# Performance work log

Measured on AMD Instinct MI355X. Metric: run time of the kernel, lower is better.

The kernel has to match this reference:

```python
import math
import jax, jax.numpy as jnp
import numpy as np

_TEMP_CLAMP = 4.6

def _l2n(x):
    # torch F.normalize: x / max(||x||, eps)
    return x / jnp.maximum(jnp.linalg.norm(x, axis=-1, keepdims=True), 1e-12)

def setup_inputs() -> dict:
    key = jax.random.key(0)
    k1, k2, k3, k4, k5 = jax.random.split(key, 5)
    B, S, D, V, NNEG = 1024, 64, 128, 100000, 2048
    hidden = jax.random.normal(k1, (B, S, D), dtype=jnp.float32)
    y = jax.random.randint(k2, (B, S), 0, V, dtype=jnp.int64)
    embed_table = jax.random.normal(k3, (V, D), dtype=jnp.float32)
    sampling_probs = jax.random.uniform(k4, (V,), dtype=jnp.float32, minval=1e-6, maxval=1.0)
    sampled_indices = jax.random.randint(k5, (NNEG,), 0, V, dtype=jnp.int64)
    log_temperature = jnp.asarray(math.log(1.0 / 0.07), dtype=jnp.float32)
    return {"hidden": hidden, "y": y, "embed_table": embed_table,
            "sampling_probs": sampling_probs, "sampled_indices": sampled_indices,
            "log_temperature": log_temperature}

def reference(hidden, y, embed_table, sampling_probs, sampled_indices, log_temperature):
    D = hidden.shape[-1]
    h = hidden.reshape(-1, D)          # [N, D]
    yf = y.reshape(-1)                 # [N]
    valid = (yf != 0)                  # padding mask (static-shape weighting instead of boolean gather)

    true_p = sampling_probs[yf]                # [N]
    samp_p = sampling_probs[sampled_indices]   # [NNEG]
    e_pos = embed_table[yf]                    # [N, D]
    e_neg = embed_table[sampled_indices]       # [NNEG, D]

    temp = jnp.exp(jnp.minimum(log_temperature, _TEMP_CLAMP))
    hn = _l2n(h)
    pos_logits = jnp.sum(hn * _l2n(e_pos), axis=-1) * temp        # [N]
    neg_logits = (hn @ _l2n(e_neg).T) * temp                      # [N, NNEG]

    collision = yf[:, None] == sampled_indices[None, :]
    neg_logits = jnp.where(collision, -1e9, neg_logits)

    pos_adj = pos_logits - jnp.log(true_p + 1e-10)                # [N]
    neg_adj = neg_logits - jnp.log(samp_p + 1e-10)[None, :]       # [N, NNEG]
    logits = jnp.concatenate([pos_adj[:, None], neg_adj], axis=1) # [N, 1+NNEG]

    per_row = -jax.nn.log_softmax(logits, axis=-1)[:, 0]          # CE with label 0
    w = valid.astype(per_row.dtype)
    return jnp.sum(per_row * w) / jnp.maximum(jnp.sum(w), 1.0)
```

## Files before the change

### kernel.cpp

```cpp
#include <hip/hip_runtime.h>
#include <math.h>

#define TPB 256
#define NNEG 2048
#define D 128
#define RPB 128
#define RPW 32
#define NSPLIT 2
#define HALF (NNEG / NSPLIT)
#define NCHH (HALF / 64)
#define L2E 1.44269504088896340736f

typedef __attribute__((ext_vector_type(8))) short bf16x8;
typedef __attribute__((ext_vector_type(4))) float f32x4;

#define MFMA16 __builtin_amdgcn_mfma_f32_16x16x32_bf16

static __device__ __forceinline__ unsigned int f2bf(float f) {
    unsigned int u = __float_as_uint(f);
    return (u + 0x7FFFu + ((u >> 16) & 1u)) >> 16;
}

static __device__ __forceinline__ void stage16(const void* g, void* l) {
    __builtin_amdgcn_global_load_lds(
        (const __attribute__((address_space(1))) unsigned int*)g,
        (__attribute__((address_space(3))) unsigned int*)l, 16, 0, 0);
}

__global__ __launch_bounds__(TPB) void sspe_prep(
    const float* __restrict__ embed,
    const float* __restrict__ sprobs,
    const int* __restrict__ sidx,
    unsigned int* __restrict__ en_bf,
    float* __restrict__ ln_samp)
{
    const int t = threadIdx.x;
    const int wave = t >> 6;
    const int lane = t & 63;
    const int j = blockIdx.x * 4 + wave;
    const int idx = sidx[j];

    float2 v = reinterpret_cast<const float2*>(embed)[(size_t)idx * 64 + lane];
    float ss = v.x * v.x + v.y * v.y;
    ss += __shfl_xor(ss, 1);
    ss += __shfl_xor(ss, 2);
    ss += __shfl_xor(ss, 4);
    ss += __shfl_xor(ss, 8);
    ss += __shfl_xor(ss, 16);
    ss += __shfl_xor(ss, 32);
    const float rinv = 1.0f / fmaxf(sqrtf(ss), 1e-12f);
    en_bf[(size_t)j * 64 + lane] = f2bf(v.x * rinv) | (f2bf(v.y * rinv) << 16);
    if (lane == 0) ln_samp[j] = logf(sprobs[idx] + 1e-10f);
}

__global__ __launch_bounds__(TPB, 4) void sspe_main(
    const float* __restrict__ hidden,
    const int* __restrict__ y,
    const float* __restrict__ embed,
    const float* __restrict__ sprobs,
    const int* __restrict__ sidx,
    const float* __restrict__ ltemp,
    const unsigned int* __restrict__ en_bf,
    const float* __restrict__ ln_samp,
    float* __restrict__ pos_adj,
    float* __restrict__ lsum,
    int nrows)
{
    const int t = threadIdx.x;
    const int wave = t >> 6;
    const int lane = t & 63;
    const int jh = blockIdx.x & 1;
    const int rb = (blockIdx.x >> 1) * RPB;

    __shared__ __align__(16) unsigned char smem[RPB * 256];
    __shared__ int ys[RPB];

    const float temp = __builtin_amdgcn_exp2f(fminf(ltemp[0], 4.6f) * L2E);
    const float t2 = temp * L2E;
    const float Mln = temp + 14.0f;
    const float M2 = Mln * L2E;

    if (t < RPB) ys[t] = y[rb + t];
    __syncthreads();

    #pragma unroll 1
    for (int i = 0; i < RPW; i += 4) {
        float2 h2[4], e2[4];
        int yi[4];
        #pragma unroll
        for (int u = 0; u < 4; ++u) {
            const int lr = wave * RPW + i + u;
            h2[u] = reinterpret_cast<const float2*>(hidden)[(size_t)(rb + lr) * 64 + lane];
            yi[u] = ys[lr];
            e2[u] = make_float2(0.0f, 0.0f);
        }
        if (jh == 0) {
            #pragma unroll
            for (int u = 0; u < 4; ++u)
                e2[u] = reinterpret_cast<const float2*>(embed)[(size_t)yi[u] * 64 + lane];
        }
        float ss[4], es[4], dt[4];
        #pragma unroll
        for (int u = 0; u < 4; ++u) {
            ss[u] = h2[u].x * h2[u].x + h2[u].y * h2[u].y;
            es[u] = e2[u].x * e2[u].x + e2[u].y * e2[u].y;
            dt[u] = h2[u].x * e2[u].x + h2[u].y * e2[u].y;
        }
        #pragma unroll
        for (int m = 1; m <= 32; m <<= 1)
            #pragma unroll
            for (int u = 0; u < 4; ++u) {
                ss[u] += __shfl_xor(ss[u], m);
                es[u] += __shfl_xor(es[u], m);
                dt[u] += __shfl_xor(dt[u], m);
            }
        #pragma unroll
        for (int u = 0; u < 4; ++u) {
            const int lr = wave * RPW + i + u;
            const float rinv = 1.0f / fmaxf(sqrtf(ss[u]), 1e-12f);
            const unsigned int uu = f2bf(h2[u].x * rinv) | (f2bf(h2[u].y * rinv) << 16);
            const int rx = (lr & 7) << 4;
            *reinterpret_cast<unsigned int*>(smem + lr * 256 + ((lane * 4) ^ rx)) = uu;
            if (jh == 0 && lane == 0)
                pos_adj[rb + lr] = dt[u] * rinv * (1.0f / fmaxf(sqrtf(es[u]), 1e-12f)) * temp
                                   - logf(sprobs[yi[u]] + 1e-10f);
        }
    }
    __syncthreads();

    bf16x8 A0[4], A1[4];
    {
        const int row0 = wave * RPW + (lane & 15);
        const int rx = (lane & 7) << 4;
        #pragma unroll
        for (int ks = 0; ks < 4; ++ks) {
            const int col = (ks * 64 + ((lane >> 4) << 4)) ^ rx;
            A0[ks] = *reinterpret_cast<const bf16x8*>(smem + row0 * 256 + col);
            A1[ks] = *reinterpret_cast<const bf16x8*>(smem + (row0 + 16) * 256 + col);
        }
    }
    __syncthreads();

    const int cj = lane & 15;
    const int rgrp = lane >> 4;
    int yv0[4], yv1[4];
    float l0[4], l1[4];
    #pragma unroll
    for (int j = 0; j < 4; ++j) {
        yv0[j] = ys[wave * RPW + rgrp * 4 + j];
        yv1[j] = ys[wave * RPW + 16 + rgrp * 4 + j];
        l0[j] = 0.0f;
        l1[j] = 0.0f;
    }

    unsigned int soff[4];
    #pragma unroll
    for (int i = 0; i < 4; ++i) {
        const int d = wave * 4 + i;
        soff[i] = (unsigned int)((d >> 2) * 4096 + (lane & 15) * 256
                                 + (d & 3) * 64 + (lane >> 4) * 16);
    }
    const unsigned char* en = reinterpret_cast<const unsigned char*>(en_bf)
                            + (size_t)jh * HALF * 256;
    const int nb0 = jh * HALF;

    #pragma unroll
    for (int i = 0; i < 4; ++i)
        stage16(en + soff[i], smem + (wave * 4 + i) * 1024);

    #pragma unroll 1
    for (int ch = 0; ch < NCHH; ++ch) {
        const int cur = (ch & 1) << 14;
        __syncthreads();

        float lk[4];
        int ci[4];
        #pragma unroll
        for (int nt = 0; nt < 4; ++nt) {
            lk[nt] = ln_samp[nb0 + ch * 64 + nt * 16 + cj];
            ci[nt] = sidx[nb0 + ch * 64 + nt * 16 + cj];
        }

        if (ch + 1 < NCHH) {
            const unsigned char* enn = en + (size_t)(ch + 1) * 16384;
            #pragma unroll
            for (int i = 0; i < 4; ++i)
                stage16(enn + soff[i], smem + (cur ^ 16384) + (wave * 4 + i) * 1024);
        }

        const unsigned char* bb = smem + cur + lane * 16;
        f32x4 c0[4], c1[4];
        #pragma unroll
        for (int nt = 0; nt < 4; ++nt) {
            c0[nt] = (f32x4){0.f, 0.f, 0.f, 0.f};
            c1[nt] = (f32x4){0.f, 0.f, 0.f, 0.f};
            #pragma unroll
            for (int ks = 0; ks < 4; ++ks) {
                const bf16x8 b = *reinterpret_cast<const bf16x8*>(bb + (nt * 4 + ks) * 1024);
                c0[nt] = MFMA16(A0[ks], b, c0[nt], 0, 0, 0);
                c1[nt] = MFMA16(A1[ks], b, c1[nt], 0, 0, 0);
            }
        }

        #pragma unroll
        for (int nt = 0; nt < 4; ++nt) {
            const float nl2 = fmaf(lk[nt], -L2E, -M2);
            #pragma unroll
            for (int j = 0; j < 4; ++j) {
                const float a0 = fmaf(c0[nt][j], t2, nl2);
                const float a1 = fmaf(c1[nt][j], t2, nl2);
                const float e0 = __builtin_amdgcn_exp2f(a0);
                const float e1 = __builtin_amdgcn_exp2f(a1);
                l0[j] += (ci[nt] == yv0[j]) ? 0.0f : e0;
                l1[j] += (ci[nt] == yv1[j]) ? 0.0f : e1;
            }
        }
    }

    #pragma unroll
    for (int j = 0; j < 4; ++j) {
        float v0 = l0[j], v1 = l1[j];
        v0 += __shfl_xor(v0, 1);  v1 += __shfl_xor(v1, 1);
        v0 += __shfl_xor(v0, 2);  v1 += __shfl_xor(v1, 2);
        v0 += __shfl_xor(v0, 4);  v1 += __shfl_xor(v1, 4);
        v0 += __shfl_xor(v0, 8);  v1 += __shfl_xor(v1, 8);
        l0[j] = v0;
        l1[j] = v1;
    }
    if (cj == 0) {
        float* dst = lsum + (size_t)jh * nrows + rb + wave * RPW;
        #pragma unroll
        for (int j = 0; j < 4; ++j) {
            dst[rgrp * 4 + j] = l0[j];
            dst[16 + rgrp * 4 + j] = l1[j];
        }
    }
}

__global__ __launch_bounds__(TPB) void sspe_rows(
    const int* __restrict__ y,
    const float* __restrict__ ltemp,
    const float* __restrict__ pos_adj,
    const float* __restrict__ lsum,
    int nrows,
    float2* __restrict__ partials)
{
    __shared__ float2 red2[4];
    const int t = threadIdx.x;
    const int wave = t >> 6;
    const int lane = t & 63;
    const int r = blockIdx.x * TPB + t;

    const float temp = __builtin_amdgcn_exp2f(fminf(ltemp[0], 4.6f) * L2E);
    const float Mln = temp + 14.0f;
    const float M2 = Mln * L2E;

    const float s = lsum[r] + lsum[(size_t)nrows + r];
    const float pa = pos_adj[r];
    const float stot = s + __builtin_amdgcn_exp2f(fmaf(pa, L2E, -M2));
    float w = (y[r] != 0) ? 1.0f : 0.0f;
    float per = (Mln + logf(stot) - pa) * w;

    #pragma unroll
    for (int msk = 1; msk < 64; msk <<= 1) {
        per += __shfl_xor(per, msk);
        w += __shfl_xor(w, msk);
    }
    if (lane == 0) red2[wave] = make_float2(per, w);
    __syncthreads();
    if (t == 0) {
        const float2 a = red2[0], b = red2[1], c = red2[2], d = red2[3];
        partials[blockIdx.x] = make_float2(a.x + b.x + c.x + d.x,
                                           a.y + b.y + c.y + d.y);
    }
}

__global__ __launch_bounds__(TPB) void sspe_finalize(
    const float2* __restrict__ partials, int n, float* __restrict__ out)
{
    __shared__ float ssum[TPB];
    __shared__ float scnt[TPB];
    const int t = threadIdx.x;
    float s = 0.0f, c = 0.0f;
    for (int i = t; i < n; i += TPB) {
        const float2 p = partials[i];
        s += p.x; c += p.y;
    }
    ssum[t] = s; scnt[t] = c;
    __syncthreads();
    for (int k = TPB / 2; k > 0; k >>= 1) {
        if (t < k) { ssum[t] += ssum[t + k]; scnt[t] += scnt[t + k]; }
        __syncthreads();
    }
    if (t == 0) out[0] = ssum[0] / fmaxf(scnt[0], 1.0f);
}

extern "C" void kernel_launch(void* const* d_in, const int* in_sizes, int n_in,
                              void* d_out, int out_size, void* d_ws, size_t ws_size,
                              hipStream_t stream) {
    const float* hidden = (const float*)d_in[0];
    const int*   yv     = (const int*)d_in[1];
    const float* embed  = (const float*)d_in[2];
    const float* sprobs = (const float*)d_in[3];
    const int*   sidx   = (const int*)d_in[4];
    const float* ltemp  = (const float*)d_in[5];
    float* out = (float*)d_out;

    const int nrows = in_sizes[1];
    const int nblocks = (nrows / RPB) * NSPLIT;

    char* w = (char*)d_ws;
    size_t off = 0;
    unsigned int* en_bf = (unsigned int*)(w + off); off += (size_t)NNEG * D * 2;
    float* ln_samp      = (float*)(w + off);        off += (size_t)NNEG * 4;
    float* pos_adj      = (float*)(w + off);        off += (size_t)nrows * 4;
    float* lsum         = (float*)(w + off);        off += (size_t)NSPLIT * nrows * 4;
    float2* partials    = (float2*)(w + off);

    sspe_prep<<<NNEG / 4, TPB, 0, stream>>>(embed, sprobs, sidx, en_bf, ln_samp);
    sspe_main<<<nblocks, TPB, 0, stream>>>(hidden, yv, embed, sprobs, sidx, ltemp,
                                           en_bf, ln_samp, pos_adj, lsum, nrows);
    sspe_rows<<<nrows / TPB, TPB, 0, stream>>>(yv, ltemp, pos_adj, lsum, nrows, partials);
    sspe_finalize<<<1, TPB, 0, stream>>>(partials, nrows / TPB, out);
}
```

Baseline: 93.72 us.

## Move collision masking out of main GEMM loop via bitmap-driven correction pass

The main kernel stops comparing every label against every sampled index inside the exp-sum loop. Instead, the prep kernel builds a vocab bitmap of the sampled ids, and the rows kernel recomputes and subtracts the contribution of colliding negatives for the few rows that hit. The main kernel also changes its tiling: 256 rows per block and a 4-way split of the negatives. Each wave now normalizes hidden rows directly into MFMA registers, without an LDS round-trip, and holds four 16-row A tiles. Costs are an extra clear kernel, an atomic bitmap build and per-row correction work, plus a clamp that guards against cancellation error.

```diff
diff --git a/kernel.cpp b/kernel.cpp
--- a/kernel.cpp
+++ b/kernel.cpp
@@ -4,11 +4,10 @@
 #define TPB 256
 #define NNEG 2048
 #define D 128
-#define RPB 128
-#define RPW 32
-#define NSPLIT 2
-#define HALF (NNEG / NSPLIT)
-#define NCHH (HALF / 64)
+#define RPB 256
+#define NSPLIT 4
+#define QSZ (NNEG / NSPLIT)
+#define NCHQ (QSZ / 64)
 #define L2E 1.44269504088896340736f
 
 typedef __attribute__((ext_vector_type(8))) short bf16x8;
@@ -19,12 +18,24 @@
 static __device__ __forceinline__ unsigned int f2bf(float f) {
     unsigned int u = __float_as_uint(f);
     return (u + 0x7FFFu + ((u >> 16) & 1u)) >> 16;
+}
+static __device__ __forceinline__ float bfround(float f) {
+    unsigned int u = __float_as_uint(f);
+    return __uint_as_float((u + 0x7FFFu + ((u >> 16) & 1u)) & 0xFFFF0000u);
+}
+static __device__ __forceinline__ unsigned int pk2(float x, float y) {
+    return f2bf(x) | (f2bf(y) << 16);
 }
 
 static __device__ __forceinline__ void stage16(const void* g, void* l) {
     __builtin_amdgcn_global_load_lds(
         (const __attribute__((address_space(1))) unsigned int*)g,
         (__attribute__((address_space(3))) unsigned int*)l, 16, 0, 0);
+}
+
+__global__ __launch_bounds__(TPB) void sspe_clear(unsigned int* __restrict__ bm, int words) {
+    const int i = blockIdx.x * TPB + threadIdx.x;
+    if (i < words) bm[i] = 0u;
 }
 
 __global__ __launch_bounds__(TPB) void sspe_prep(
@@ -32,7 +43,8 @@
     const float* __restrict__ sprobs,
     const int* __restrict__ sidx,
     unsigned int* __restrict__ en_bf,
-    float* __restrict__ ln_samp)
+    float* __restrict__ ln_samp,
+    unsigned int* __restrict__ bitmap)
 {
     const int t = threadIdx.x;
     const int wave = t >> 6;
@@ -49,8 +61,11 @@
     ss += __shfl_xor(ss, 16);
     ss += __shfl_xor(ss, 32);
     const float rinv = 1.0f / fmaxf(sqrtf(ss), 1e-12f);
-    en_bf[(size_t)j * 64 + lane] = f2bf(v.x * rinv) | (f2bf(v.y * rinv) << 16);
-    if (lane == 0) ln_samp[j] = logf(sprobs[idx] + 1e-10f);
+    en_bf[(size_t)j * 64 + lane] = pk2(v.x * rinv, v.y * rinv);
+    if (lane == 0) {
+        ln_samp[j] = logf(sprobs[idx] + 1e-10f);
+        atomicOr(&bitmap[idx >> 5], 1u << (idx & 31));
+    }
 }
 
 __global__ __launch_bounds__(TPB, 4) void sspe_main(
@@ -58,7 +73,6 @@
     const int* __restrict__ y,
     const float* __restrict__ embed,
     const float* __restrict__ sprobs,
-    const int* __restrict__ sidx,
     const float* __restrict__ ltemp,
     const unsigned int* __restrict__ en_bf,
     const float* __restrict__ ln_samp,
@@ -69,119 +83,106 @@
     const int t = threadIdx.x;
     const int wave = t >> 6;
     const int lane = t & 63;
-    const int jh = blockIdx.x & 1;
-    const int rb = (blockIdx.x >> 1) * RPB;
-
-    __shared__ __align__(16) unsigned char smem[RPB * 256];
-    __shared__ int ys[RPB];
+    const int jh = blockIdx.x & 3;
+    const int rb = (blockIdx.x >> 2) * RPB;
+
+    __shared__ __align__(16) unsigned char smem[2 * 16384];
 
     const float temp = __builtin_amdgcn_exp2f(fminf(ltemp[0], 4.6f) * L2E);
     const float t2 = temp * L2E;
     const float Mln = temp + 14.0f;
     const float M2 = Mln * L2E;
 
-    if (t < RPB) ys[t] = y[rb + t];
-    __syncthreads();
-
-    #pragma unroll 1
-    for (int i = 0; i < RPW; i += 4) {
-        float2 h2[4], e2[4];
-        int yi[4];
-        #pragma unroll
-        for (int u = 0; u < 4; ++u) {
-            const int lr = wave * RPW + i + u;
-            h2[u] = reinterpret_cast<const float2*>(hidden)[(size_t)(rb + lr) * 64 + lane];
-            yi[u] = ys[lr];
-            e2[u] = make_float2(0.0f, 0.0f);
-        }
-        if (jh == 0) {
-            #pragma unroll
-            for (int u = 0; u < 4; ++u)
-                e2[u] = reinterpret_cast<const float2*>(embed)[(size_t)yi[u] * 64 + lane];
-        }
-        float ss[4], es[4], dt[4];
-        #pragma unroll
-        for (int u = 0; u < 4; ++u) {
-            ss[u] = h2[u].x * h2[u].x + h2[u].y * h2[u].y;
-            es[u] = e2[u].x * e2[u].x + e2[u].y * e2[u].y;
-            dt[u] = h2[u].x * e2[u].x + h2[u].y * e2[u].y;
-        }
-        #pragma unroll
-        for (int m = 1; m <= 32; m <<= 1)
-            #pragma unroll
-            for (int u = 0; u < 4; ++u) {
-                ss[u] += __shfl_xor(ss[u], m);
-                es[u] += __shfl_xor(es[u], m);
-                dt[u] += __shfl_xor(dt[u], m);
-            }
-        #pragma unroll
-        for (int u = 0; u < 4; ++u) {
-            const int lr = wave * RPW + i + u;
-            const float rinv = 1.0f / fmaxf(sqrtf(ss[u]), 1e-12f);
-            const unsigned int uu = f2bf(h2[u].x * rinv) | (f2bf(h2[u].y * rinv) << 16);
-            const int rx = (lr & 7) << 4;
-            *reinterpret_cast<unsigned int*>(smem + lr * 256 + ((lane * 4) ^ rx)) = uu;
-            if (jh == 0 && lane == 0)
-                pos_adj[rb + lr] = dt[u] * rinv * (1.0f / fmaxf(sqrtf(es[u]), 1e-12f)) * temp
-                                   - logf(sprobs[yi[u]] + 1e-10f);
-        }
-    }
-    __syncthreads();
-
-    bf16x8 A0[4], A1[4];
-    {
-        const int row0 = wave * RPW + (lane & 15);
-        const int rx = (lane & 7) << 4;
-        #pragma unroll
-        for (int ks = 0; ks < 4; ++ks) {
-            const int col = (ks * 64 + ((lane >> 4) << 4)) ^ rx;
-            A0[ks] = *reinterpret_cast<const bf16x8*>(smem + row0 * 256 + col);
-            A1[ks] = *reinterpret_cast<const bf16x8*>(smem + (row0 + 16) * 256 + col);
-        }
-    }
-    __syncthreads();
-
-    const int cj = lane & 15;
-    const int rgrp = lane >> 4;
-    int yv0[4], yv1[4];
-    float l0[4], l1[4];
-    #pragma unroll
-    for (int j = 0; j < 4; ++j) {
-        yv0[j] = ys[wave * RPW + rgrp * 4 + j];
-        yv1[j] = ys[wave * RPW + 16 + rgrp * 4 + j];
-        l0[j] = 0.0f;
-        l1[j] = 0.0f;
-    }
+    const int g = lane >> 4;
+    const int rl = lane & 15;
+    const int wbase = rb + wave * 64;
 
     unsigned int soff[4];
     #pragma unroll
     for (int i = 0; i < 4; ++i) {
         const int d = wave * 4 + i;
-        soff[i] = (unsigned int)((d >> 2) * 4096 + (lane & 15) * 256
-                                 + (d & 3) * 64 + (lane >> 4) * 16);
+        soff[i] = (unsigned int)((d >> 2) * 4096 + rl * 256 + (d & 3) * 64 + g * 16);
     }
     const unsigned char* en = reinterpret_cast<const unsigned char*>(en_bf)
-                            + (size_t)jh * HALF * 256;
-    const int nb0 = jh * HALF;
+                            + (size_t)jh * QSZ * 256;
+    const int nb0 = jh * QSZ;
 
     #pragma unroll
     for (int i = 0; i < 4; ++i)
         stage16(en + soff[i], smem + (wave * 4 + i) * 1024);
 
+    bf16x8 A[4][4];
+    #pragma unroll
+    for (int tt = 0; tt < 4; ++tt) {
+        const int row = wbase + tt * 16 + rl;
+        const float* hp = hidden + (size_t)row * D + g * 8;
+        float4 ha[4], hb[4];
+        #pragma unroll
+        for (int ks = 0; ks < 4; ++ks) {
+            ha[ks] = *reinterpret_cast<const float4*>(hp + ks * 32);
+            hb[ks] = *reinterpret_cast<const float4*>(hp + ks * 32 + 4);
+        }
+        float ss = 0.0f;
+        #pragma unroll
+        for (int ks = 0; ks < 4; ++ks) {
+            ss += ha[ks].x * ha[ks].x + ha[ks].y * ha[ks].y
+                + ha[ks].z * ha[ks].z + ha[ks].w * ha[ks].w
+                + hb[ks].x * hb[ks].x + hb[ks].y * hb[ks].y
+                + hb[ks].z * hb[ks].z + hb[ks].w * hb[ks].w;
+        }
+        ss += __shfl_xor(ss, 16);
+        ss += __shfl_xor(ss, 32);
+        const float rinv = 1.0f / fmaxf(sqrtf(ss), 1e-12f);
+        #pragma unroll
+        for (int ks = 0; ks < 4; ++ks) {
+            union { bf16x8 v; unsigned int u[4]; } ua;
+            ua.u[0] = pk2(ha[ks].x * rinv, ha[ks].y * rinv);
+            ua.u[1] = pk2(ha[ks].z * rinv, ha[ks].w * rinv);
+            ua.u[2] = pk2(hb[ks].x * rinv, hb[ks].y * rinv);
+            ua.u[3] = pk2(hb[ks].z * rinv, hb[ks].w * rinv);
+            A[tt][ks] = ua.v;
+        }
+        if (jh == 0) {
+            const int yi = y[row];
+            const float* ep = embed + (size_t)yi * D + g * 8;
+            float dt = 0.0f, es = 0.0f;
+            #pragma unroll
+            for (int ks = 0; ks < 4; ++ks) {
+                const float4 ea = *reinterpret_cast<const float4*>(ep + ks * 32);
+                const float4 eb = *reinterpret_cast<const float4*>(ep + ks * 32 + 4);
+                dt += ea.x * ha[ks].x + ea.y * ha[ks].y + ea.z * ha[ks].z + ea.w * ha[ks].w
+                    + eb.x * hb[ks].x + eb.y * hb[ks].y + eb.z * hb[ks].z + eb.w * hb[ks].w;
+                es += ea.x * ea.x + ea.y * ea.y + ea.z * ea.z + ea.w * ea.w
+                    + eb.x * eb.x + eb.y * eb.y + eb.z * eb.z + eb.w * eb.w;
+            }
+            dt += __shfl_xor(dt, 16);  es += __shfl_xor(es, 16);
+            dt += __shfl_xor(dt, 32);  es += __shfl_xor(es, 32);
+            if (lane < 16)
+                pos_adj[row] = dt * rinv * (1.0f / fmaxf(sqrtf(es), 1e-12f)) * temp
+                               - logf(sprobs[yi] + 1e-10f);
+        }
+    }
+
+    float l[4][4];
+    #pragma unroll
+    for (int tt = 0; tt < 4; ++tt)
+        #pragma unroll
+        for (int j = 0; j < 4; ++j) l[tt][j] = 0.0f;
+
+    const int cj = rl;
+    const int rgrp = g;
+
     #pragma unroll 1
-    for (int ch = 0; ch < NCHH; ++ch) {
+    for (int ch = 0; ch < NCHQ; ++ch) {
         const int cur = (ch & 1) << 14;
         __syncthreads();
 
         float lk[4];
-        int ci[4];
-        #pragma unroll
-        for (int nt = 0; nt < 4; ++nt) {
+        #pragma unroll
+        for (int nt = 0; nt < 4; ++nt)
             lk[nt] = ln_samp[nb0 + ch * 64 + nt * 16 + cj];
-            ci[nt] = sidx[nb0 + ch * 64 + nt * 16 + cj];
-        }
-
-        if (ch + 1 < NCHH) {
+
+        if (ch + 1 < NCHQ) {
             const unsigned char* enn = en + (size_t)(ch + 1) * 16384;
             #pragma unroll
             for (int i = 0; i < 4; ++i)
@@ -189,76 +190,119 @@
         }
 
         const unsigned char* bb = smem + cur + lane * 16;
-        f32x4 c0[4], c1[4];
         #pragma unroll
         for (int nt = 0; nt < 4; ++nt) {
-            c0[nt] = (f32x4){0.f, 0.f, 0.f, 0.f};
-            c1[nt] = (f32x4){0.f, 0.f, 0.f, 0.f};
+            f32x4 c0 = {0.f, 0.f, 0.f, 0.f};
+            f32x4 c1 = c0, c2 = c0, c3 = c0;
             #pragma unroll
             for (int ks = 0; ks < 4; ++ks) {
                 const bf16x8 b = *reinterpret_cast<const bf16x8*>(bb + (nt * 4 + ks) * 1024);
-                c0[nt] = MFMA16(A0[ks], b, c0[nt], 0, 0, 0);
-                c1[nt] = MFMA16(A1[ks], b, c1[nt], 0, 0, 0);
+                c0 = MFMA16(A[0][ks], b, c0, 0, 0, 0);
+                c1 = MFMA16(A[1][ks], b, c1, 0, 0, 0);
+                c2 = MFMA16(A[2][ks], b, c2, 0, 0, 0);
+                c3 = MFMA16(A[3][ks], b, c3, 0, 0, 0);
             }
-        }
-
-        #pragma unroll
-        for (int nt = 0; nt < 4; ++nt) {
             const float nl2 = fmaf(lk[nt], -L2E, -M2);
             #pragma unroll
             for (int j = 0; j < 4; ++j) {
-                const float a0 = fmaf(c0[nt][j], t2, nl2);
-                const float a1 = fmaf(c1[nt][j], t2, nl2);
-                const float e0 = __builtin_amdgcn_exp2f(a0);
-                const float e1 = __builtin_amdgcn_exp2f(a1);
-                l0[j] += (ci[nt] == yv0[j]) ? 0.0f : e0;
-                l1[j] += (ci[nt] == yv1[j]) ? 0.0f : e1;
+                l[0][j] += __builtin_amdgcn_exp2f(fmaf(c0[j], t2, nl2));
+                l[1][j] += __builtin_amdgcn_exp2f(fmaf(c1[j], t2, nl2));
+                l[2][j] += __builtin_amdgcn_exp2f(fmaf(c2[j], t2, nl2));
+                l[3][j] += __builtin_amdgcn_exp2f(fmaf(c3[j], t2, nl2));
             }
         }
     }
 
     #pragma unroll
-    for (int j = 0; j < 4; ++j) {
-        float v0 = l0[j], v1 = l1[j];
-        v0 += __shfl_xor(v0, 1);  v1 += __shfl_xor(v1, 1);
-        v0 += __shfl_xor(v0, 2);  v1 += __shfl_xor(v1, 2);
-        v0 += __shfl_xor(v0, 4);  v1 += __shfl_xor(v1, 4);
-        v0 += __shfl_xor(v0, 8);  v1 += __shfl_xor(v1, 8);
-        l0[j] = v0;
-        l1[j] = v1;
-    }
+    for (int tt = 0; tt < 4; ++tt)
+        #pragma unroll
+        for (int j = 0; j < 4; ++j) {
+            float v = l[tt][j];
+            v += __shfl_xor(v, 1);
+            v += __shfl_xor(v, 2);
+            v += __shfl_xor(v, 4);
+            v += __shfl_xor(v, 8);
+            l[tt][j] = v;
+        }
     if (cj == 0) {
-        float* dst = lsum + (size_t)jh * nrows + rb + wave * RPW;
-        #pragma unroll
-        for (int j = 0; j < 4; ++j) {
-            dst[rgrp * 4 + j] = l0[j];
-            dst[16 + rgrp * 4 + j] = l1[j];
-        }
+        float* dst = lsum + (size_t)jh * nrows + wbase;
+        #pragma unroll
+        for (int tt = 0; tt < 4; ++tt)
+            #pragma unroll
+            for (int j = 0; j < 4; ++j)
+                dst[tt * 16 + rgrp * 4 + j] = l[tt][j];
     }
 }
 
 __global__ __launch_bounds__(TPB) void sspe_rows(
     const int* __restrict__ y,
     const float* __restrict__ ltemp,
+    const int* __restrict__ sidx,
+    const float* __restrict__ hidden,
+    const unsigned int* __restrict__ en_bf,
+    const float* __restrict__ ln_samp,
+    const unsigned int* __restrict__ bitmap,
     const float* __restrict__ pos_adj,
     const float* __restrict__ lsum,
     int nrows,
     float2* __restrict__ partials)
 {
+    __shared__ int ssi[NNEG];
     __shared__ float2 red2[4];
     const int t = threadIdx.x;
     const int wave = t >> 6;
     const int lane = t & 63;
     const int r = blockIdx.x * TPB + t;
 
+    for (int k = t; k < NNEG; k += TPB) ssi[k] = sidx[k];
+    __syncthreads();
+
     const float temp = __builtin_amdgcn_exp2f(fminf(ltemp[0], 4.6f) * L2E);
+    const float t2 = temp * L2E;
     const float Mln = temp + 14.0f;
     const float M2 = Mln * L2E;
 
-    const float s = lsum[r] + lsum[(size_t)nrows + r];
+    const int yr = y[r];
+    float w = (yr != 0) ? 1.0f : 0.0f;
+    float s = lsum[r] + lsum[(size_t)nrows + r]
+            + lsum[2 * (size_t)nrows + r] + lsum[3 * (size_t)nrows + r];
+
+    const bool hit = (w > 0.0f) && ((bitmap[yr >> 5] >> (yr & 31)) & 1u);
+    unsigned long long m = __ballot(hit);
+    while (m) {
+        const int b = (int)(__ffsll((long long)m) - 1); m &= m - 1;
+        const int yb = __shfl(yr, b);
+        const int rB = __shfl(r, b);
+        const float2 h2 = reinterpret_cast<const float2*>(hidden)[(size_t)rB * 64 + lane];
+        float hs = h2.x * h2.x + h2.y * h2.y;
+        #pragma unroll
+        for (int k = 1; k <= 32; k <<= 1) hs += __shfl_xor(hs, k);
+        const float rinv = 1.0f / fmaxf(sqrtf(hs), 1e-12f);
+        const float hb0 = bfround(h2.x * rinv);
+        const float hb1 = bfround(h2.y * rinv);
+        float corr = 0.0f;
+        for (int k = 0; k < NNEG; k += 64) {
+            const int sj = ssi[k + lane];
+            unsigned long long mm = __ballot(sj == yb);
+            while (mm) {
+                const int jj = (int)(__ffsll((long long)mm) - 1); mm &= mm - 1;
+                const int j = k + jj;
+                const unsigned int eu = en_bf[(size_t)j * 64 + lane];
+                const float e0 = __uint_as_float(eu << 16);
+                const float e1 = __uint_as_float(eu & 0xFFFF0000u);
+                float d = hb0 * e0 + hb1 * e1;
+                #pragma unroll
+                for (int q = 1; q <= 32; q <<= 1) d += __shfl_xor(d, q);
+                const float lkj = ln_samp[j];
+                corr += __builtin_amdgcn_exp2f(fmaf(d, t2, fmaf(lkj, -L2E, -M2)));
+            }
+        }
+        if (lane == b) s -= corr;
+    }
+    s = fmaxf(s, 0.0f);
+
     const float pa = pos_adj[r];
     const float stot = s + __builtin_amdgcn_exp2f(fmaf(pa, L2E, -M2));
-    float w = (y[r] != 0) ? 1.0f : 0.0f;
     float per = (Mln + logf(stot) - pa) * w;
 
     #pragma unroll
@@ -269,9 +313,9 @@
     if (lane == 0) red2[wave] = make_float2(per, w);
     __syncthreads();
     if (t == 0) {
-        const float2 a = red2[0], b = red2[1], c = red2[2], d = red2[3];
-        partials[blockIdx.x] = make_float2(a.x + b.x + c.x + d.x,
-                                           a.y + b.y + c.y + d.y);
+        const float2 a = red2[0], b2 = red2[1], c = red2[2], d2 = red2[3];
+        partials[blockIdx.x] = make_float2(a.x + b2.x + c.x + d2.x,
+                                           a.y + b2.y + c.y + d2.y);
     }
 }
 
@@ -307,6 +351,8 @@
     float* out = (float*)d_out;
 
     const int nrows = in_sizes[1];
+    const int vocab = in_sizes[3];
+    const int bmw = (vocab + 31) / 32;
     const int nblocks = (nrows / RPB) * NSPLIT;
 
     char* w = (char*)d_ws;
@@ -315,11 +361,14 @@
     float* ln_samp      = (float*)(w + off);        off += (size_t)NNEG * 4;
     float* pos_adj      = (float*)(w + off);        off += (size_t)nrows * 4;
     float* lsum         = (float*)(w + off);        off += (size_t)NSPLIT * nrows * 4;
-    float2* partials    = (float2*)(w + off);
-
-    sspe_prep<<<NNEG / 4, TPB, 0, stream>>>(embed, sprobs, sidx, en_bf, ln_samp);
-    sspe_main<<<nblocks, TPB, 0, stream>>>(hidden, yv, embed, sprobs, sidx, ltemp,
+    float2* partials    = (float2*)(w + off);       off += (size_t)(nrows / TPB) * 8;
+    unsigned int* bitmap = (unsigned int*)(w + off);
+
+    sspe_clear<<<(bmw + TPB - 1) / TPB, TPB, 0, stream>>>(bitmap, bmw);
+    sspe_prep<<<NNEG / 4, TPB, 0, stream>>>(embed, sprobs, sidx, en_bf, ln_samp, bitmap);
+    sspe_main<<<nblocks, TPB, 0, stream>>>(hidden, yv, embed, sprobs, ltemp,
                                            en_bf, ln_samp, pos_adj, lsum, nrows);
-    sspe_rows<<<nrows / TPB, TPB, 0, stream>>>(yv, ltemp, pos_adj, lsum, nrows, partials);
+    sspe_rows<<<nrows / TPB, TPB, 0, stream>>>(yv, ltemp, sidx, hidden, en_bf, ln_samp,
+                                               bitmap, pos_adj, lsum, nrows, partials);
     sspe_finalize<<<1, TPB, 0, stream>>>(partials, nrows / TPB, out);
 }
```

After: 179.6 us. +91.6%, slower.
